# Kernel tuning notes

Hardware: AMD Instinct MI355X
Metric: run time of the kernel (lower is better)

Reference implementation:

```python
import jax, jax.numpy as jnp
from jax import lax
import numpy as np

EPS_DENOM = 1e-5
EPS_NCC = 1e-5
HIGH = 0.5  # IntensityNormalization(high=0.5): min-max rescale of weights to [0, high]


def _box_conv(v, kernel):
    # Dense ones-kernel 3D box filter, VALID padding, stride 1 (NCDHW / OIDHW).
    return lax.conv_general_dilated(
        v, kernel, window_strides=(1, 1, 1), padding='VALID',
        dimension_numbers=('NCDHW', 'OIDHW', 'NCDHW'))


def setup_inputs() -> dict:
    key = jax.random.key(0)
    k1, k2 = jax.random.split(key)
    shape = (2, 1, 160, 192, 160)
    y_pred = jax.random.normal(k1, shape, dtype=jnp.float32)
    y_true = jax.random.normal(k2, shape, dtype=jnp.float32)
    kernel = jnp.ones((1, 1, 7, 7, 7), dtype=jnp.float32)
    return {"y_pred": y_pred, "y_true": y_true, "kernel": kernel}


def reference(y_pred, y_true, kernel):
    nw = kernel.sum()  # = 343 for a 7^3 ones kernel
    x, y = y_pred, y_true
    sum_x = _box_conv(x, kernel)
    sum_y = _box_conv(y, kernel)
    sum_x2 = _box_conv(x * x, kernel)
    sum_y2 = _box_conv(y * y, kernel)
    sum_xy = _box_conv(x * y, kernel)

    mean_x = sum_x / nw
    mean_y = sum_y / nw
    num = sum_xy + mean_x * mean_y * nw - mean_x * sum_y - mean_y * sum_x
    denom_0 = mean_x * mean_x * nw + sum_x2 - 2.0 * mean_x * sum_x
    denom_1 = mean_y * mean_y * nw + sum_y2 - 2.0 * mean_y * sum_y
    denom = denom_0 * denom_1

    valid = denom > EPS_DENOM
    safe_denom = jnp.where(valid, denom, 1.0)
    ncc = jnp.where(valid, num / jnp.sqrt(safe_denom), 0.0)
    invalid = (ncc < -1.0 - EPS_NCC) | (ncc > 1.0 + EPS_NCC)
    ncc = jnp.where(invalid, 0.0, ncc)
    all_valid = valid & ~invalid

    # Intensity normalization of weights: min-max rescale of local variance sum
    # over the valid voxels to [0, HIGH], then normalize to sum to 1.
    v = 0.5 * (denom_0 + denom_1)
    vmin = jnp.min(jnp.where(all_valid, v, jnp.inf))
    vmax = jnp.max(jnp.where(all_valid, v, -jnp.inf))
    w = jnp.where(all_valid, (v - vmin) / (vmax - vmin + 1e-12) * HIGH, 0.0)
    w = w / w.sum()

    return 1.0 - jnp.sum(jnp.where(all_valid, ncc, 0.0) * w)
```

## Files before the change

### kernel.cpp

```cpp
#include <hip/hip_runtime.h>
#include <math.h>

#define NN 2
#define DD 160
#define HH 192
#define WW 160
#define DO 154
#define HO 186
#define WO 154

#define NWO 3
#define NHO 47
#define ZCH 8
#define ZOC 20
#define NB (NWO * NHO * NN * ZCH)

#define LDS_SYNC() do { __builtin_amdgcn_s_waitcnt(0xC07F); __builtin_amdgcn_s_barrier(); } while (0)

__device__ __forceinline__ float block_sum(float v, float* sm) {
  int tid = threadIdx.x;
  sm[tid] = v;
  __syncthreads();
#pragma unroll
  for (int off = 128; off > 0; off >>= 1) {
    if (tid < off) sm[tid] += sm[tid + off];
    __syncthreads();
  }
  float r = sm[0];
  __syncthreads();
  return r;
}

__device__ __forceinline__ float block_min(float v, float* sm) {
  int tid = threadIdx.x;
  sm[tid] = v;
  __syncthreads();
#pragma unroll
  for (int off = 128; off > 0; off >>= 1) {
    if (tid < off) sm[tid] = fminf(sm[tid], sm[tid + off]);
    __syncthreads();
  }
  float r = sm[0];
  __syncthreads();
  return r;
}

__global__ __launch_bounds__(256, 4) void ncc_fused(const float* __restrict__ X,
                                                    const float* __restrict__ Y,
                                                    float* __restrict__ part) {
  __shared__ __align__(16) float R[5][10][64];
  __shared__ __align__(16) float Mh[5][4][64];
  __shared__ float sm[256];

  const int tid = threadIdx.x;
  const int tx = tid & 63, ty = tid >> 6;
  const int wo0 = blockIdx.x * 64;
  const int ho0 = blockIdx.y * 4;
  const int n   = blockIdx.z >> 3;
  const int ck  = blockIdx.z & 7;
  const int z0  = ck * ZOC;
  const int zout = min(ZOC, DO - z0);
  const int nslice = zout + 6;

  const int wo = wo0 + tx, ho = ho0 + ty;
  const bool act = (wo < WO) && (ho < HO);

  const size_t slice = (size_t)HH * WW;
  const float* Xn = X + (size_t)n * DD * slice;
  const float* Yn = Y + (size_t)n * DD * slice;
  const float inv_nw = 1.0f / 343.0f;
  const float LO = -1.0f - 1e-5f, HI = 1.0f + 1e-5f;

  const int pA  = tid;
  const bool hasA = (pA < 160);
  const int rA  = pA >> 4;
  const int cqA = (pA & 15) << 2;
  const int hA  = ho0 + rA;
  const int baseW = wo0 + cqA;
  const bool okA  = hasA && (hA < HH) && (baseW < WO);
  const bool tail = okA && (baseW + 9 >= WW);
  const float* XrowA = Xn + (size_t)hA * WW + baseW;
  const float* YrowA = Yn + (size_t)hA * WW + baseW;

  float4 lx0 = {0,0,0,0}, lx1 = {0,0,0,0}, ly0 = {0,0,0,0}, ly1 = {0,0,0,0};
  float2 lx2 = {0,0}, ly2 = {0,0};

  auto loadA = [&](int s_in) {
    if (okA) {
      const float* xp = XrowA + (size_t)(z0 + s_in) * slice;
      const float* yp = YrowA + (size_t)(z0 + s_in) * slice;
      lx0 = *(const float4*)xp; lx1 = *(const float4*)(xp + 4);
      ly0 = *(const float4*)yp; ly1 = *(const float4*)(yp + 4);
      if (!tail) { lx2 = *(const float2*)(xp + 8); ly2 = *(const float2*)(yp + 8); }
      else       { lx2 = make_float2(0.f, 0.f);    ly2 = make_float2(0.f, 0.f); }
    }
  };

  auto storeA = [&]() {
    if (okA) {
      float x0=lx0.x,x1=lx0.y,x2=lx0.z,x3=lx0.w,x4=lx1.x,x5=lx1.y,x6=lx1.z,x7=lx1.w,x8=lx2.x,x9=lx2.y;
      float y0=ly0.x,y1=ly0.y,y2=ly0.z,y3=ly0.w,y4=ly1.x,y5=ly1.y,y6=ly1.z,y7=ly1.w,y8=ly2.x,y9=ly2.y;
      {
        float a = x0+x1+x2+x3+x4+x5+x6;
        float b = a - x0 + x7, c = b - x1 + x8, d = c - x2 + x9;
        *(float4*)&R[0][rA][cqA] = make_float4(a, b, c, d);
      }
      {
        float a = y0+y1+y2+y3+y4+y5+y6;
        float b = a - y0 + y7, c = b - y1 + y8, d = c - y2 + y9;
        *(float4*)&R[1][rA][cqA] = make_float4(a, b, c, d);
      }
      {
        float a = x0*x0+x1*x1+x2*x2+x3*x3+x4*x4+x5*x5+x6*x6;
        float b = a - x0*x0 + x7*x7, c = b - x1*x1 + x8*x8, d = c - x2*x2 + x9*x9;
        *(float4*)&R[2][rA][cqA] = make_float4(a, b, c, d);
      }
      {
        float a = y0*y0+y1*y1+y2*y2+y3*y3+y4*y4+y5*y5+y6*y6;
        float b = a - y0*y0 + y7*y7, c = b - y1*y1 + y8*y8, d = c - y2*y2 + y9*y9;
        *(float4*)&R[3][rA][cqA] = make_float4(a, b, c, d);
      }
      {
        float a = x0*y0+x1*y1+x2*y2+x3*y3+x4*y4+x5*y5+x6*y6;
        float b = a - x0*y0 + x7*y7, c = b - x1*y1 + x8*y8, d = c - x2*y2 + x9*y9;
        *(float4*)&R[4][rA][cqA] = make_float4(a, b, c, d);
      }
    }
  };

  auto phaseH = [&]() {
    {
      const int ch = ty, w = tx;
      const float* rp = &R[ch][0][w];
      float r0=rp[0],r1=rp[64],r2=rp[128],r3=rp[192],r4=rp[256],
            r5=rp[320],r6=rp[384],r7=rp[448],r8=rp[512],r9=rp[576];
      float m0 = r0+r1+r2+r3+r4+r5+r6;
      float m1 = m0 - r0 + r7, m2 = m1 - r1 + r8, m3 = m2 - r2 + r9;
      Mh[ch][0][w]=m0; Mh[ch][1][w]=m1; Mh[ch][2][w]=m2; Mh[ch][3][w]=m3;
    }
    if (tx < 16) {
      const int w = ty * 16 + tx;
      const float* rp = &R[4][0][w];
      float r0=rp[0],r1=rp[64],r2=rp[128],r3=rp[192],r4=rp[256],
            r5=rp[320],r6=rp[384],r7=rp[448],r8=rp[512],r9=rp[576];
      float m0 = r0+r1+r2+r3+r4+r5+r6;
      float m1 = m0 - r0 + r7, m2 = m1 - r1 + r8, m3 = m2 - r2 + r9;
      Mh[4][0][w]=m0; Mh[4][1][w]=m1; Mh[4][2][w]=m2; Mh[4][3][w]=m3;
    }
  };

  float a0[7], a1[7], a2[7], a3[7], a4[7];
#pragma unroll
  for (int j = 0; j < 7; ++j) { a0[j]=0.f; a1[j]=0.f; a2[j]=0.f; a3[j]=0.f; a4[j]=0.f; }
  float p_snv = 0.f, p_sn = 0.f, p_sv = 0.f, p_cnt = 0.f, p_vmin = 3.4e38f;

  loadA(0);
  storeA();
  __syncthreads();

  for (int sb = 0; sb < nslice; sb += 7) {
#pragma unroll
    for (int u = 0; u < 7; ++u) {
      const int s = sb + u;
      if (s < nslice) {
        if (s + 1 < nslice) loadA(s + 1);
        phaseH();
        LDS_SYNC();
        {
          float m0 = Mh[0][ty][tx], m1 = Mh[1][ty][tx], m2 = Mh[2][ty][tx],
                m3 = Mh[3][ty][tx], m4 = Mh[4][ty][tx];
#pragma unroll
          for (int j = 0; j < 7; ++j) {
            a0[j]+=m0; a1[j]+=m1; a2[j]+=m2; a3[j]+=m3; a4[j]+=m4;
          }
          if (s >= 6 && act) {
            float zs0=a0[u], zs1=a1[u], zs2=a2[u], zs3=a3[u], zs4=a4[u];
            float num = zs4 - zs0 * zs1 * inv_nw;
            float d0  = zs2 - zs0 * zs0 * inv_nw;
            float d1  = zs3 - zs1 * zs1 * inv_nw;
            float den = d0 * d1;
            if (den > 1e-5f) {
              float ncc = num * __frsqrt_rn(den);
              if (ncc >= LO && ncc <= HI) {
                float v = 0.5f * (d0 + d1);
                p_snv += ncc * v; p_sn += ncc; p_sv += v; p_cnt += 1.f;
                p_vmin = fminf(p_vmin, v);
              }
            }
          }
          a0[u]=0.f; a1[u]=0.f; a2[u]=0.f; a3[u]=0.f; a4[u]=0.f;
        }
        if (s + 1 < nslice) storeA();
        LDS_SYNC();
      }
    }
  }

  float bsnv = block_sum(p_snv, sm);
  float bsn  = block_sum(p_sn, sm);
  float bsv  = block_sum(p_sv, sm);
  float bcnt = block_sum(p_cnt, sm);
  float bmin = block_min(p_vmin, sm);
  if (tid == 0) {
    const int bid = blockIdx.x + NWO * (blockIdx.y + NHO * blockIdx.z);
    float* pp = part + (size_t)bid * 8;
    pp[0] = bsnv; pp[1] = bsn; pp[2] = bsv; pp[3] = bcnt; pp[4] = bmin;
  }
}

__global__ __launch_bounds__(256) void fin(const float* __restrict__ part,
                                           float* __restrict__ out) {
  __shared__ float sm[256];
  const int tid = threadIdx.x;
  float s0 = 0.f, s1 = 0.f, s2 = 0.f, s3 = 0.f, vm = 3.4e38f;
  for (int b = tid; b < NB; b += 256) {
    const float* pp = part + (size_t)b * 8;
    s0 += pp[0]; s1 += pp[1]; s2 += pp[2]; s3 += pp[3];
    vm = fminf(vm, pp[4]);
  }
  s0 = block_sum(s0, sm);
  s1 = block_sum(s1, sm);
  s2 = block_sum(s2, sm);
  s3 = block_sum(s3, sm);
  vm = block_min(vm, sm);
  if (tid == 0) {
    out[0] = 1.0f - (s0 - vm * s1) / (s2 - vm * s3);
  }
}

extern "C" void kernel_launch(void* const* d_in, const int* in_sizes, int n_in,
                              void* d_out, int out_size, void* d_ws, size_t ws_size,
                              hipStream_t stream) {
  const float* X = (const float*)d_in[0];
  const float* Y = (const float*)d_in[1];

  float* part = (float*)d_ws;

  dim3 g(NWO, NHO, NN * ZCH);
  ncc_fused<<<g, 256, 0, stream>>>(X, Y, part);
  fin<<<1, 256, 0, stream>>>(part, (float*)d_out);
}
```

Before: 178.2 us.

## Enlarge H tile to 8 rows, use running z-sums, and wave-shuffle reductions

Each block now covers 8 output rows instead of 4, and each thread loads 14 columns and produces 8 sliding W-sums, so the 6-row and 6-column halo reloads are spread over more outputs. The 7-deep per-slice z accumulator arrays are replaced by a running sum with a history ring, cutting the per-slice additions. The final block reductions use wave shuffles instead of LDS tree loops. The cost is more registers per thread (occupancy hint lowered from 4 to 3), and only 112 threads do the load stage, so load work is less evenly spread across the block.

```diff
diff --git a/kernel.cpp b/kernel.cpp
--- a/kernel.cpp
+++ b/kernel.cpp
@@ -10,7 +10,8 @@
 #define WO 154
 
 #define NWO 3
-#define NHO 47
+#define HOT 8
+#define NHO 24
 #define ZCH 8
 #define ZOC 20
 #define NB (NWO * NHO * NN * ZCH)
@@ -45,25 +46,52 @@
   return r;
 }
 
-__global__ __launch_bounds__(256, 4) void ncc_fused(const float* __restrict__ X,
+__device__ __forceinline__ float wave_sum(float v) {
+  v += __shfl_xor(v, 32); v += __shfl_xor(v, 16); v += __shfl_xor(v, 8);
+  v += __shfl_xor(v, 4);  v += __shfl_xor(v, 2);  v += __shfl_xor(v, 1);
+  return v;
+}
+
+__device__ __forceinline__ float wave_min(float v) {
+  v = fminf(v, __shfl_xor(v, 32)); v = fminf(v, __shfl_xor(v, 16));
+  v = fminf(v, __shfl_xor(v, 8));  v = fminf(v, __shfl_xor(v, 4));
+  v = fminf(v, __shfl_xor(v, 2));  v = fminf(v, __shfl_xor(v, 1));
+  return v;
+}
+
+#define SLIDE7(V, M) do { \
+  float s0 = ((V[0]+V[1])+(V[2]+V[3])) + ((V[4]+V[5])+V[6]); \
+  float s1 = s0 - V[0] + V[7]; \
+  float s2 = s1 - V[1] + V[8]; \
+  float s3 = s2 - V[2] + V[9]; \
+  float s4 = s3 - V[3] + V[10]; \
+  float s5 = s4 - V[4] + V[11]; \
+  float s6 = s5 - V[5] + V[12]; \
+  float s7 = s6 - V[6] + V[13]; \
+  *(float4*)&R[M][0][rA][c4] = make_float4(s0, s1, s2, s3); \
+  *(float4*)&R[M][1][rA][c4] = make_float4(s4, s5, s6, s7); \
+} while (0)
+
+__global__ __launch_bounds__(256, 3) void ncc_fused(const float* __restrict__ X,
                                                     const float* __restrict__ Y,
                                                     float* __restrict__ part) {
-  __shared__ __align__(16) float R[5][10][64];
-  __shared__ __align__(16) float Mh[5][4][64];
-  __shared__ float sm[256];
+  __shared__ __align__(16) float R[5][2][14][64];
+  __shared__ __align__(16) float Mh[5][HOT][64];
+  __shared__ float red[4][5];
 
   const int tid = threadIdx.x;
   const int tx = tid & 63, ty = tid >> 6;
   const int wo0 = blockIdx.x * 64;
-  const int ho0 = blockIdx.y * 4;
+  const int ho0 = blockIdx.y * HOT;
   const int n   = blockIdx.z >> 3;
   const int ck  = blockIdx.z & 7;
   const int z0  = ck * ZOC;
   const int zout = min(ZOC, DO - z0);
   const int nslice = zout + 6;
 
-  const int wo = wo0 + tx, ho = ho0 + ty;
-  const bool act = (wo < WO) && (ho < HO);
+  const int wo = wo0 + tx;
+  const bool act0 = (wo < WO) && (ho0 + ty < HO);
+  const bool act1 = (wo < WO) && (ho0 + ty + 4 < HO);
 
   const size_t slice = (size_t)HH * WW;
   const float* Xn = X + (size_t)n * DD * slice;
@@ -72,86 +100,95 @@
   const float LO = -1.0f - 1e-5f, HI = 1.0f + 1e-5f;
 
   const int pA  = tid;
-  const bool hasA = (pA < 160);
-  const int rA  = pA >> 4;
-  const int cqA = (pA & 15) << 2;
+  const bool hasA = (pA < 112);
+  const int rA  = pA >> 3;
+  const int c8  = (pA & 7) << 3;
+  const int c4  = (pA & 7) << 2;
   const int hA  = ho0 + rA;
-  const int baseW = wo0 + cqA;
+  const int baseW = wo0 + c8;
   const bool okA  = hasA && (hA < HH) && (baseW < WO);
-  const bool tail = okA && (baseW + 9 >= WW);
+  const bool tail = okA && (baseW + 14 > WW);
   const float* XrowA = Xn + (size_t)hA * WW + baseW;
   const float* YrowA = Yn + (size_t)hA * WW + baseW;
 
-  float4 lx0 = {0,0,0,0}, lx1 = {0,0,0,0}, ly0 = {0,0,0,0}, ly1 = {0,0,0,0};
-  float2 lx2 = {0,0}, ly2 = {0,0};
+  float4 lx0={0,0,0,0}, lx1={0,0,0,0}, lx2={0,0,0,0};
+  float4 ly0={0,0,0,0}, ly1={0,0,0,0}, ly2={0,0,0,0};
+  float2 lx3={0,0}, ly3={0,0};
 
   auto loadA = [&](int s_in) {
     if (okA) {
       const float* xp = XrowA + (size_t)(z0 + s_in) * slice;
       const float* yp = YrowA + (size_t)(z0 + s_in) * slice;
-      lx0 = *(const float4*)xp; lx1 = *(const float4*)(xp + 4);
-      ly0 = *(const float4*)yp; ly1 = *(const float4*)(yp + 4);
-      if (!tail) { lx2 = *(const float2*)(xp + 8); ly2 = *(const float2*)(yp + 8); }
-      else       { lx2 = make_float2(0.f, 0.f);    ly2 = make_float2(0.f, 0.f); }
+      lx0 = *(const float4*)xp;       lx1 = *(const float4*)(xp + 4);
+      ly0 = *(const float4*)yp;       ly1 = *(const float4*)(yp + 4);
+      if (!tail) {
+        lx2 = *(const float4*)(xp + 8); lx3 = *(const float2*)(xp + 12);
+        ly2 = *(const float4*)(yp + 8); ly3 = *(const float2*)(yp + 12);
+      } else {
+        lx2 = make_float4(0.f,0.f,0.f,0.f); lx3 = make_float2(0.f,0.f);
+        ly2 = make_float4(0.f,0.f,0.f,0.f); ly3 = make_float2(0.f,0.f);
+      }
     }
   };
 
   auto storeA = [&]() {
     if (okA) {
-      float x0=lx0.x,x1=lx0.y,x2=lx0.z,x3=lx0.w,x4=lx1.x,x5=lx1.y,x6=lx1.z,x7=lx1.w,x8=lx2.x,x9=lx2.y;
-      float y0=ly0.x,y1=ly0.y,y2=ly0.z,y3=ly0.w,y4=ly1.x,y5=ly1.y,y6=ly1.z,y7=ly1.w,y8=ly2.x,y9=ly2.y;
+      const float x[14] = {lx0.x,lx0.y,lx0.z,lx0.w, lx1.x,lx1.y,lx1.z,lx1.w,
+                           lx2.x,lx2.y,lx2.z,lx2.w, lx3.x,lx3.y};
+      const float y[14] = {ly0.x,ly0.y,ly0.z,ly0.w, ly1.x,ly1.y,ly1.z,ly1.w,
+                           ly2.x,ly2.y,ly2.z,ly2.w, ly3.x,ly3.y};
+      SLIDE7(x, 0);
+      SLIDE7(y, 1);
       {
-        float a = x0+x1+x2+x3+x4+x5+x6;
-        float b = a - x0 + x7, c = b - x1 + x8, d = c - x2 + x9;
-        *(float4*)&R[0][rA][cqA] = make_float4(a, b, c, d);
+        float t[14];
+#pragma unroll
+        for (int i = 0; i < 14; ++i) t[i] = x[i] * x[i];
+        SLIDE7(t, 2);
       }
       {
-        float a = y0+y1+y2+y3+y4+y5+y6;
-        float b = a - y0 + y7, c = b - y1 + y8, d = c - y2 + y9;
-        *(float4*)&R[1][rA][cqA] = make_float4(a, b, c, d);
+        float t[14];
+#pragma unroll
+        for (int i = 0; i < 14; ++i) t[i] = y[i] * y[i];
+        SLIDE7(t, 3);
       }
       {
-        float a = x0*x0+x1*x1+x2*x2+x3*x3+x4*x4+x5*x5+x6*x6;
-        float b = a - x0*x0 + x7*x7, c = b - x1*x1 + x8*x8, d = c - x2*x2 + x9*x9;
-        *(float4*)&R[2][rA][cqA] = make_float4(a, b, c, d);
-      }
-      {
-        float a = y0*y0+y1*y1+y2*y2+y3*y3+y4*y4+y5*y5+y6*y6;
-        float b = a - y0*y0 + y7*y7, c = b - y1*y1 + y8*y8, d = c - y2*y2 + y9*y9;
-        *(float4*)&R[3][rA][cqA] = make_float4(a, b, c, d);
-      }
-      {
-        float a = x0*y0+x1*y1+x2*y2+x3*y3+x4*y4+x5*y5+x6*y6;
-        float b = a - x0*y0 + x7*y7, c = b - x1*y1 + x8*y8, d = c - x2*y2 + x9*y9;
-        *(float4*)&R[4][rA][cqA] = make_float4(a, b, c, d);
+        float t[14];
+#pragma unroll
+        for (int i = 0; i < 14; ++i) t[i] = x[i] * y[i];
+        SLIDE7(t, 4);
       }
     }
   };
 
+  auto phaseHitem = [&](int ch, int w) {
+    const int q = w >> 3, j = w & 7;
+    const float* rp = &R[ch][j >> 2][0][(q << 2) + (j & 3)];
+    float r0=rp[0],   r1=rp[64],  r2=rp[128], r3=rp[192], r4=rp[256],
+          r5=rp[320], r6=rp[384], r7=rp[448], r8=rp[512], r9=rp[576],
+          r10=rp[640], r11=rp[704], r12=rp[768], r13=rp[832];
+    float m0 = ((r0+r1)+(r2+r3)) + ((r4+r5)+r6);
+    float m1 = m0 - r0 + r7;
+    float m2 = m1 - r1 + r8;
+    float m3 = m2 - r2 + r9;
+    float m4 = m3 - r3 + r10;
+    float m5 = m4 - r4 + r11;
+    float m6 = m5 - r5 + r12;
+    float m7 = m6 - r6 + r13;
+    Mh[ch][0][w]=m0; Mh[ch][1][w]=m1; Mh[ch][2][w]=m2; Mh[ch][3][w]=m3;
+    Mh[ch][4][w]=m4; Mh[ch][5][w]=m5; Mh[ch][6][w]=m6; Mh[ch][7][w]=m7;
+  };
   auto phaseH = [&]() {
-    {
-      const int ch = ty, w = tx;
-      const float* rp = &R[ch][0][w];
-      float r0=rp[0],r1=rp[64],r2=rp[128],r3=rp[192],r4=rp[256],
-            r5=rp[320],r6=rp[384],r7=rp[448],r8=rp[512],r9=rp[576];
-      float m0 = r0+r1+r2+r3+r4+r5+r6;
-      float m1 = m0 - r0 + r7, m2 = m1 - r1 + r8, m3 = m2 - r2 + r9;
-      Mh[ch][0][w]=m0; Mh[ch][1][w]=m1; Mh[ch][2][w]=m2; Mh[ch][3][w]=m3;
-    }
-    if (tx < 16) {
-      const int w = ty * 16 + tx;
-      const float* rp = &R[4][0][w];
-      float r0=rp[0],r1=rp[64],r2=rp[128],r3=rp[192],r4=rp[256],
-            r5=rp[320],r6=rp[384],r7=rp[448],r8=rp[512],r9=rp[576];
-      float m0 = r0+r1+r2+r3+r4+r5+r6;
-      float m1 = m0 - r0 + r7, m2 = m1 - r1 + r8, m3 = m2 - r2 + r9;
-      Mh[4][0][w]=m0; Mh[4][1][w]=m1; Mh[4][2][w]=m2; Mh[4][3][w]=m3;
-    }
-  };
-
-  float a0[7], a1[7], a2[7], a3[7], a4[7];
-#pragma unroll
-  for (int j = 0; j < 7; ++j) { a0[j]=0.f; a1[j]=0.f; a2[j]=0.f; a3[j]=0.f; a4[j]=0.f; }
+    phaseHitem(ty, tx);
+    if (tid < 64) phaseHitem(4, tid);
+  };
+
+  float zs0[2]={0,0}, zs1[2]={0,0}, zs2[2]={0,0}, zs3[2]={0,0}, zs4[2]={0,0};
+  float h0[2][7], h1[2][7], h2[2][7], h3[2][7], h4[2][7];
+#pragma unroll
+  for (int j = 0; j < 7; ++j) {
+    h0[0][j]=0.f; h1[0][j]=0.f; h2[0][j]=0.f; h3[0][j]=0.f; h4[0][j]=0.f;
+    h0[1][j]=0.f; h1[1][j]=0.f; h2[1][j]=0.f; h3[1][j]=0.f; h4[1][j]=0.f;
+  }
   float p_snv = 0.f, p_sn = 0.f, p_sv = 0.f, p_cnt = 0.f, p_vmin = 3.4e38f;
 
   loadA(0);
@@ -167,28 +204,31 @@
         phaseH();
         LDS_SYNC();
         {
-          float m0 = Mh[0][ty][tx], m1 = Mh[1][ty][tx], m2 = Mh[2][ty][tx],
-                m3 = Mh[3][ty][tx], m4 = Mh[4][ty][tx];
-#pragma unroll
-          for (int j = 0; j < 7; ++j) {
-            a0[j]+=m0; a1[j]+=m1; a2[j]+=m2; a3[j]+=m3; a4[j]+=m4;
-          }
-          if (s >= 6 && act) {
-            float zs0=a0[u], zs1=a1[u], zs2=a2[u], zs3=a3[u], zs4=a4[u];
-            float num = zs4 - zs0 * zs1 * inv_nw;
-            float d0  = zs2 - zs0 * zs0 * inv_nw;
-            float d1  = zs3 - zs1 * zs1 * inv_nw;
-            float den = d0 * d1;
-            if (den > 1e-5f) {
-              float ncc = num * __frsqrt_rn(den);
-              if (ncc >= LO && ncc <= HI) {
-                float v = 0.5f * (d0 + d1);
-                p_snv += ncc * v; p_sn += ncc; p_sv += v; p_cnt += 1.f;
-                p_vmin = fminf(p_vmin, v);
+#pragma unroll
+          for (int rb = 0; rb < 2; ++rb) {
+            const int row = ty + (rb << 2);
+            float m0 = Mh[0][row][tx], m1 = Mh[1][row][tx], m2 = Mh[2][row][tx],
+                  m3 = Mh[3][row][tx], m4 = Mh[4][row][tx];
+            zs0[rb] += m0 - h0[rb][u]; h0[rb][u] = m0;
+            zs1[rb] += m1 - h1[rb][u]; h1[rb][u] = m1;
+            zs2[rb] += m2 - h2[rb][u]; h2[rb][u] = m2;
+            zs3[rb] += m3 - h3[rb][u]; h3[rb][u] = m3;
+            zs4[rb] += m4 - h4[rb][u]; h4[rb][u] = m4;
+            if (s >= 6 && (rb ? act1 : act0)) {
+              float num = zs4[rb] - zs0[rb] * zs1[rb] * inv_nw;
+              float d0  = zs2[rb] - zs0[rb] * zs0[rb] * inv_nw;
+              float d1  = zs3[rb] - zs1[rb] * zs1[rb] * inv_nw;
+              float den = d0 * d1;
+              if (den > 1e-5f) {
+                float ncc = num * __frsqrt_rn(den);
+                if (ncc >= LO && ncc <= HI) {
+                  float v = 0.5f * (d0 + d1);
+                  p_snv += ncc * v; p_sn += ncc; p_sv += v; p_cnt += 1.f;
+                  p_vmin = fminf(p_vmin, v);
+                }
               }
             }
           }
-          a0[u]=0.f; a1[u]=0.f; a2[u]=0.f; a3[u]=0.f; a4[u]=0.f;
         }
         if (s + 1 < nslice) storeA();
         LDS_SYNC();
@@ -196,15 +236,24 @@
     }
   }
 
-  float bsnv = block_sum(p_snv, sm);
-  float bsn  = block_sum(p_sn, sm);
-  float bsv  = block_sum(p_sv, sm);
-  float bcnt = block_sum(p_cnt, sm);
-  float bmin = block_min(p_vmin, sm);
+  float r0 = wave_sum(p_snv);
+  float r1 = wave_sum(p_sn);
+  float r2 = wave_sum(p_sv);
+  float r3 = wave_sum(p_cnt);
+  float r4 = wave_min(p_vmin);
+  if (tx == 0) {
+    red[ty][0]=r0; red[ty][1]=r1; red[ty][2]=r2; red[ty][3]=r3; red[ty][4]=r4;
+  }
+  __syncthreads();
   if (tid == 0) {
+    float s0 = (red[0][0]+red[1][0]) + (red[2][0]+red[3][0]);
+    float s1 = (red[0][1]+red[1][1]) + (red[2][1]+red[3][1]);
+    float s2 = (red[0][2]+red[1][2]) + (red[2][2]+red[3][2]);
+    float s3 = (red[0][3]+red[1][3]) + (red[2][3]+red[3][3]);
+    float s4 = fminf(fminf(red[0][4],red[1][4]), fminf(red[2][4],red[3][4]));
     const int bid = blockIdx.x + NWO * (blockIdx.y + NHO * blockIdx.z);
     float* pp = part + (size_t)bid * 8;
-    pp[0] = bsnv; pp[1] = bsn; pp[2] = bsv; pp[3] = bcnt; pp[4] = bmin;
+    pp[0] = s0; pp[1] = s1; pp[2] = s2; pp[3] = s3; pp[4] = s4;
   }
 }
 
```

Measured after the change: 164.8 us. -7.5%, faster.
